# Kernel tuning notes

Hardware: AMD Instinct MI355X
Metric: run time of the kernel (lower is better)

The kernel has to match this reference:

```python
import jax, jax.numpy as jnp
import numpy as np

B, S, D = 1024, 192, 512
MAX_ITEMS, NUM_LAYERS = 64, 3
LN_EPS = 1e-5


def setup_inputs() -> dict:
    key = jax.random.key(0)
    k_tok, k_pad, k_item, k_layer, k_temp = jax.random.split(key, 5)
    token_embeddings = jax.random.normal(k_tok, (B, S, D), dtype=jnp.float32)
    # Left-padded mask: zeros then contiguous ones until the end of the row.
    pad_len = jax.random.randint(k_pad, (B,), 0, S)  # at least 1 real token
    attention_mask = (jnp.arange(S)[None, :] >= pad_len[:, None]).astype(jnp.int32)
    item_pos_emb = 0.01 * jax.random.normal(k_item, (MAX_ITEMS, D), dtype=jnp.float32)
    layer_emb = 0.01 * jax.random.normal(k_layer, (NUM_LAYERS, D), dtype=jnp.float32)
    temporal_decay = 0.02 * jax.random.normal(k_temp, (MAX_ITEMS, D), dtype=jnp.float32)
    ln_weight = jnp.ones((D,), dtype=jnp.float32)
    ln_bias = jnp.zeros((D,), dtype=jnp.float32)
    return {
        "token_embeddings": token_embeddings,
        "attention_mask": attention_mask,
        "item_pos_emb": item_pos_emb,
        "layer_emb": layer_emb,
        "temporal_decay": temporal_decay,
        "ln_weight": ln_weight,
        "ln_bias": ln_bias,
    }


def reference(token_embeddings, attention_mask, item_pos_emb, layer_emb,
              temporal_decay, ln_weight, ln_bias):
    mask = attention_mask > 0                              # (B, S) bool
    has_content = jnp.any(mask, axis=1)                    # (B,)
    start = jnp.argmax(mask, axis=1)                       # first non-pad index
    end = S - jnp.argmax(mask[:, ::-1], axis=1)            # last non-pad index + 1
    idx = jnp.arange(S)[None, :]                           # (1, S)
    pos = idx - start[:, None]                             # content-relative position
    in_range = (pos >= 0) & (idx < end[:, None]) & has_content[:, None]
    pos_c = jnp.clip(pos, 0)
    item_idx = jnp.where(in_range, pos_c // NUM_LAYERS, 0)  # (B, S)
    layer_idx = jnp.where(in_range, pos_c % NUM_LAYERS, 0)
    add = item_pos_emb[item_idx] + layer_emb[layer_idx] + temporal_decay[item_idx]
    enhanced = token_embeddings + jnp.where(in_range[..., None], add, 0.0)
    # LayerNorm over last dim
    mu = jnp.mean(enhanced, axis=-1, keepdims=True)
    var = jnp.mean(jnp.square(enhanced - mu), axis=-1, keepdims=True)
    normed = (enhanced - mu) * jax.lax.rsqrt(var + LN_EPS) * ln_weight + ln_bias
    # zero out padding (dropout is identity in eval mode)
    return normed * attention_mask[..., None].astype(normed.dtype)
```

## Files before the change

### kernel.cpp

```cpp
#include <hip/hip_runtime.h>

typedef float f4 __attribute__((ext_vector_type(4)));

#define BB 1024
#define SS 192
#define DD 512
#define NUM_LAYERS 3
#define LN_EPS 1e-5f
#define NROWS (BB * SS)
#define FUSED_BLOCKS 2048
#define NWAVES (FUSED_BLOCKS * 4)
#define NITER (NROWS / NWAVES)

__global__ __launch_bounds__(256) void prep_kernel(
    const int* __restrict__ mask,
    const float* __restrict__ item_pos,
    const float* __restrict__ layer_emb,
    const float* __restrict__ decay,
    float* __restrict__ add_tab,
    int* __restrict__ start)
{
    if (blockIdx.x < SS) {
        const int p = blockIdx.x;
        const int t = threadIdx.x;
        if (t < DD / 4) {
            const int item = p / NUM_LAYERS;
            const int layer = p - item * NUM_LAYERS;
            const f4 iv = reinterpret_cast<const f4*>(item_pos + item * DD)[t];
            const f4 lv = reinterpret_cast<const f4*>(layer_emb + layer * DD)[t];
            const f4 dv = reinterpret_cast<const f4*>(decay + item * DD)[t];
            reinterpret_cast<f4*>(add_tab + p * DD)[t] = iv + lv + dv;
        }
    } else {
        const int b = (blockIdx.x - SS) * 4 + (threadIdx.x >> 6);
        const int lane = threadIdx.x & 63;
        if (b < BB) {
            const int* m = mask + b * SS;
            const unsigned long long b0 = __ballot(m[lane] > 0);
            const unsigned long long b1 = __ballot(m[lane + 64] > 0);
            const unsigned long long b2 = __ballot(m[lane + 128] > 0);
            int idx;
            if (b0)      idx = __ffsll(b0) - 1;
            else if (b1) idx = 64 + __ffsll(b1) - 1;
            else if (b2) idx = 128 + __ffsll(b2) - 1;
            else         idx = SS;
            if (lane == 0) start[b] = idx;
        }
    }
}

__device__ __forceinline__ float wave_allreduce(float v, int xaddr32) {
    v += __uint_as_float((unsigned)__builtin_amdgcn_update_dpp(
            0, (int)__float_as_uint(v), 0xB1, 0xF, 0xF, true));
    v += __uint_as_float((unsigned)__builtin_amdgcn_update_dpp(
            0, (int)__float_as_uint(v), 0x4E, 0xF, 0xF, true));
    v += __uint_as_float((unsigned)__builtin_amdgcn_update_dpp(
            0, (int)__float_as_uint(v), 0x141, 0xF, 0xF, true));
    v += __uint_as_float((unsigned)__builtin_amdgcn_update_dpp(
            0, (int)__float_as_uint(v), 0x140, 0xF, 0xF, true));
    v += __uint_as_float((unsigned)__builtin_amdgcn_ds_swizzle(
            (int)__float_as_uint(v), 0x401f));
    v += __uint_as_float((unsigned)__builtin_amdgcn_ds_bpermute(
            xaddr32, (int)__float_as_uint(v)));
    return v;
}

__global__ __launch_bounds__(256) void fused_kernel(
    const float* __restrict__ tok,
    const float* __restrict__ add_tab,
    const float* __restrict__ lnw,
    const float* __restrict__ lnb,
    const int* __restrict__ start,
    float* __restrict__ out)
{
    const int wid = threadIdx.x >> 6;
    const int lane = threadIdx.x & 63;
    const int l0 = lane;
    const int l1 = lane + 64;
    const int xaddr32 = (lane ^ 32) << 2;

    const f4 w0 = reinterpret_cast<const f4*>(lnw)[l0];
    const f4 w1 = reinterpret_cast<const f4*>(lnw)[l1];
    const f4 c0 = reinterpret_cast<const f4*>(lnb)[l0];
    const f4 c1 = reinterpret_cast<const f4*>(lnb)[l1];

    const int wave = blockIdx.x * 4 + wid;

    #pragma unroll 1
    for (int row = wave; row < NROWS; row += NWAVES) {
        const int b = row / SS;
        const int s = row - b * SS;
        const int st = start[b];

        f4* o4 = reinterpret_cast<f4*>(out + (size_t)row * DD);

        if (s < st) {
            const f4 z = {0.f, 0.f, 0.f, 0.f};
            o4[l0] = z;
            o4[l1] = z;
            continue;
        }

        const int pos = s - st;

        const f4* x4 = reinterpret_cast<const f4*>(tok + (size_t)row * DD);
        const f4 xv0 = x4[l0];
        const f4 xv1 = x4[l1];

        const f4* a4 = reinterpret_cast<const f4*>(add_tab + pos * DD);
        const f4 y0 = xv0 + a4[l0];
        const f4 y1 = xv1 + a4[l1];

        float sum = (y0.x + y0.y) + (y0.z + y0.w)
                  + (y1.x + y1.y) + (y1.z + y1.w);
        const f4 q0 = y0 * y0;
        const f4 q1 = y1 * y1;
        float sq = (q0.x + q0.y) + (q0.z + q0.w)
                 + (q1.x + q1.y) + (q1.z + q1.w);

        sum = wave_allreduce(sum, xaddr32);
        sq  = wave_allreduce(sq, xaddr32);

        const float mu  = sum * (1.0f / DD);
        const float var = sq * (1.0f / DD) - mu * mu;
        const float inv = rsqrtf(var + LN_EPS);

        const f4 ov0 = (y0 - mu) * inv * w0 + c0;
        const f4 ov1 = (y1 - mu) * inv * w1 + c1;
        o4[l0] = ov0;
        o4[l1] = ov1;
    }
}

extern "C" void kernel_launch(void* const* d_in, const int* in_sizes, int n_in,
                              void* d_out, int out_size, void* d_ws, size_t ws_size,
                              hipStream_t stream) {
    const float* tok       = (const float*)d_in[0];
    const int*   mask      = (const int*)d_in[1];
    const float* item_pos  = (const float*)d_in[2];
    const float* layer_emb = (const float*)d_in[3];
    const float* decay     = (const float*)d_in[4];
    const float* lnw       = (const float*)d_in[5];
    const float* lnb       = (const float*)d_in[6];
    float* out = (float*)d_out;

    float* add_tab = (float*)d_ws;
    int* start = (int*)((char*)d_ws + (size_t)SS * DD * sizeof(float));

    prep_kernel<<<SS + 256, 256, 0, stream>>>(mask, item_pos, layer_emb, decay,
                                              add_tab, start);
    fused_kernel<<<FUSED_BLOCKS, 256, 0, stream>>>(tok, add_tab, lnw, lnb, start, out);
}
```

Measured before the change: 146.4 us.

## Map two blocks per batch row and zero padding region with contiguous stores

The grid-stride loop over all rows is replaced by two blocks per batch element. Each pair of blocks first zero-fills the left padding region as one contiguous strided store, then its 8 waves process the content rows. This drops the per-row division and the repeated start lookups, and makes padding writes contiguous. The cost is load imbalance across blocks, since rows have different content lengths.

```diff
diff --git a/kernel.cpp b/kernel.cpp
--- a/kernel.cpp
+++ b/kernel.cpp
@@ -7,10 +7,6 @@
 #define DD 512
 #define NUM_LAYERS 3
 #define LN_EPS 1e-5f
-#define NROWS (BB * SS)
-#define FUSED_BLOCKS 2048
-#define NWAVES (FUSED_BLOCKS * 4)
-#define NITER (NROWS / NWAVES)
 
 __global__ __launch_bounds__(256) void prep_kernel(
     const int* __restrict__ mask,
@@ -73,37 +69,39 @@
     const int* __restrict__ start,
     float* __restrict__ out)
 {
-    const int wid = threadIdx.x >> 6;
-    const int lane = threadIdx.x & 63;
+    const int b = blockIdx.x >> 1;
+    const int half = blockIdx.x & 1;
+    const int tid = threadIdx.x;
+    const int wid = tid >> 6;
+    const int lane = tid & 63;
     const int l0 = lane;
     const int l1 = lane + 64;
     const int xaddr32 = (lane ^ 32) << 2;
+
+    const int st = start[b];
 
     const f4 w0 = reinterpret_cast<const f4*>(lnw)[l0];
     const f4 w1 = reinterpret_cast<const f4*>(lnw)[l1];
     const f4 c0 = reinterpret_cast<const f4*>(lnb)[l0];
     const f4 c1 = reinterpret_cast<const f4*>(lnb)[l1];
 
-    const int wave = blockIdx.x * 4 + wid;
+    float* const obase = out + (size_t)b * SS * DD;
+
+    {
+        f4* o4 = reinterpret_cast<f4*>(obase);
+        const int nf4 = st * (DD / 4);
+        const f4 z = {0.f, 0.f, 0.f, 0.f};
+        for (int i = half * 256 + tid; i < nf4; i += 512)
+            o4[i] = z;
+    }
+
+    const int j = half * 4 + wid;
 
     #pragma unroll 1
-    for (int row = wave; row < NROWS; row += NWAVES) {
-        const int b = row / SS;
-        const int s = row - b * SS;
-        const int st = start[b];
-
-        f4* o4 = reinterpret_cast<f4*>(out + (size_t)row * DD);
-
-        if (s < st) {
-            const f4 z = {0.f, 0.f, 0.f, 0.f};
-            o4[l0] = z;
-            o4[l1] = z;
-            continue;
-        }
-
+    for (int s = st + j; s < SS; s += 8) {
         const int pos = s - st;
 
-        const f4* x4 = reinterpret_cast<const f4*>(tok + (size_t)row * DD);
+        const f4* x4 = reinterpret_cast<const f4*>(tok + (size_t)b * SS * DD + s * DD);
         const f4 xv0 = x4[l0];
         const f4 xv1 = x4[l1];
 
@@ -125,10 +123,9 @@
         const float var = sq * (1.0f / DD) - mu * mu;
         const float inv = rsqrtf(var + LN_EPS);
 
-        const f4 ov0 = (y0 - mu) * inv * w0 + c0;
-        const f4 ov1 = (y1 - mu) * inv * w1 + c1;
-        o4[l0] = ov0;
-        o4[l1] = ov1;
+        f4* o4 = reinterpret_cast<f4*>(obase + s * DD);
+        o4[l0] = (y0 - mu) * inv * w0 + c0;
+        o4[l1] = (y1 - mu) * inv * w1 + c1;
     }
 }
 
@@ -149,5 +146,5 @@
 
     prep_kernel<<<SS + 256, 256, 0, stream>>>(mask, item_pos, layer_emb, decay,
                                               add_tab, start);
-    fused_kernel<<<FUSED_BLOCKS, 256, 0, stream>>>(tok, add_tab, lnw, lnb, start, out);
+    fused_kernel<<<BB * 2, 256, 0, stream>>>(tok, add_tab, lnw, lnb, start, out);
 }
```

New measurement: 148.7 us. No clear change (+1.6%).
